# Kernel tuning notes

Measured on AMD Instinct MI355X. Metric: run time of the kernel, lower is better.

## Reference

```python
import jax, jax.numpy as jnp
import numpy as np

BATCH, N_FEATURES, D_MODEL = 8192, 8192, 1024


def setup_inputs() -> dict:
    key = jax.random.key(0)
    kx, kw = jax.random.split(key)
    # x: sparse feature activations in the original (COO); dense uniform here.
    x = jax.random.uniform(kx, (BATCH, N_FEATURES), dtype=jnp.float32)
    # Xavier-normal init for W_tr [n_features, d_model].
    std = float(np.sqrt(2.0 / (N_FEATURES + D_MODEL)))
    W_tr = jax.random.normal(kw, (N_FEATURES, D_MODEL), dtype=jnp.float32) * std
    bias = jnp.zeros((N_FEATURES,), dtype=jnp.float32)
    return {"x": x, "W_tr": W_tr, "bias": bias}


def reference(x, W_tr, bias):
    # h = x @ W_tr              : [B, n_features] @ [n_features, d_model] -> [B, d_model]
    # out = relu(h @ W_tr.T + b): [B, d_model] @ [d_model, n_features] -> [B, n_features]
    h = jnp.einsum("bf,fd->bd", x, W_tr)
    return jax.nn.relu(jnp.einsum("bd,fd->bf", h, W_tr) + bias)
```

## Files before the change

kernel.cpp:

```cpp
#include <hip/hip_runtime.h>
#include <hip/hip_bf16.h>
#include <stdint.h>

#define BATCH  8192
#define NFEAT  8192
#define DMODEL 1024

typedef unsigned short u16;
typedef __attribute__((ext_vector_type(8))) short  short8;
typedef __attribute__((ext_vector_type(4))) float  f32x4;

__device__ __forceinline__ u16 f2b(float f) {
    uint32_t u = __float_as_uint(f);
    u += 0x7fffu + ((u >> 16) & 1u);
    return (u16)(u >> 16);
}

__device__ __forceinline__ void gld16(const u16* g, void* l) {
    __builtin_amdgcn_global_load_lds(
        (const __attribute__((address_space(1))) void*)(uintptr_t)g,
        (__attribute__((address_space(3))) void*)(uint32_t)(uintptr_t)l,
        16, 0, 0);
}


__global__ void cvt_x_kernel(const float* __restrict__ x, u16* __restrict__ xb) {
    int i = blockIdx.x * blockDim.x + threadIdx.x;
    const float4* xv = (const float4*)x;
    float4 a = xv[2 * i];
    float4 b = xv[2 * i + 1];
    union { u16 u[8]; uint4 v; } o;
    o.u[0] = f2b(a.x); o.u[1] = f2b(a.y); o.u[2] = f2b(a.z); o.u[3] = f2b(a.w);
    o.u[4] = f2b(b.x); o.u[5] = f2b(b.y); o.u[6] = f2b(b.z); o.u[7] = f2b(b.w);
    ((uint4*)xb)[i] = o.v;
}

__global__ void cvt_w_kernel(const float* __restrict__ W,
                             u16* __restrict__ wb, u16* __restrict__ wt) {
    __shared__ u16 tile[64][65];
    const int f0 = blockIdx.x * 64;
    const int d0 = blockIdx.y * 64;
    const int t  = threadIdx.x;
#pragma unroll
    for (int rep = 0; rep < 16; ++rep) {
        int idx = rep * 256 + t;
        int r = idx >> 6, c = idx & 63;
        float v = W[(size_t)(f0 + r) * DMODEL + d0 + c];
        u16 u = f2b(v);
        tile[r][c] = u;
        wb[(size_t)(f0 + r) * DMODEL + d0 + c] = u;
    }
    __syncthreads();
#pragma unroll
    for (int rep = 0; rep < 16; ++rep) {
        int idx = rep * 256 + t;
        int r = idx >> 6, c = idx & 63;
        wt[(size_t)(d0 + r) * NFEAT + f0 + c] = tile[c][r];
    }
}

#define SYNC_IN()  do { __builtin_amdgcn_sched_barrier(0); __builtin_amdgcn_s_barrier(); \
                        asm volatile("s_waitcnt lgkmcnt(0)" ::: "memory");               \
                        __builtin_amdgcn_sched_barrier(0); } while (0)
#define SYNC_OUT() do { __builtin_amdgcn_s_setprio(0); __builtin_amdgcn_sched_barrier(0); \
                        __builtin_amdgcn_s_barrier(); } while (0)

__global__ __launch_bounds__(512, 2)
void gemm1_8phase(const u16* __restrict__ A, const u16* __restrict__ B,
                  u16* __restrict__ H, int N, int K) {
    const int NT = K >> 6;
    __shared__ __align__(1024) char lds[98304];
    const int BOFF = 65536;

    const int tid  = threadIdx.x;
    const int lane = tid & 63;
    const int wave = tid >> 6;
    const int wm   = wave >> 2;
    const int wn   = wave & 3;

    const int nwg = gridDim.x;
    const int swz = (blockIdx.x & 7) * (nwg >> 3) + (blockIdx.x >> 3);
    const int ntn = N >> 7;
    const int tm0 = (swz / ntn) << 8;
    const int tn0 = (swz % ntn) << 7;

    const int srl = lane >> 2;
    const int sch = (lane & 3) ^ (((lane >> 5) & 1) << 1);
    const int scol  = (wave & 1) * 32 + sch * 8;
    const int srow0 = (wave >> 1) * 16 + srl;

    const u16* pa[2][2];
    pa[0][0] = A + (size_t)(tm0 + srow0)            * K + scol;
    pa[0][1] = A + (size_t)(tm0 + srow0 + 64)       * K + scol;
    pa[1][0] = A + (size_t)(tm0 + 128 + srow0)      * K + scol;
    pa[1][1] = A + (size_t)(tm0 + 128 + srow0 + 64) * K + scol;
    const u16* pb[2];
    pb[0] = B + (size_t)(tn0 + srow0)      * K + scol;
    pb[1] = B + (size_t)(tn0 + srow0 + 64) * K + scol;

    auto STAGE_A = [&](int tau, int half) {
        if (tau < NT) {
            char* d = lds + (tau & 1) * 32768 + half * 16384 + wave * 1024;
            gld16(pa[half][0] + (size_t)tau * 64, d);
            gld16(pa[half][1] + (size_t)tau * 64, d + 8192);
        }
    };
    auto STAGE_B = [&](int tau) {
        if (tau < NT) {
            char* d = lds + BOFF + (tau & 1) * 16384 + wave * 1024;
            gld16(pb[0] + (size_t)tau * 64, d);
            gld16(pb[1] + (size_t)tau * 64, d + 8192);
        }
    };

    const int l15 = lane & 15, lhi = lane >> 4;
    const int pch = lhi ^ (((lane >> 3) & 1) << 1);
    const int lof = l15 * 64 + pch * 16;

    short8 a[4][2];
    short8 b[2][2];
    f32x4  acc[8][2] = {};

    const char* Ab;
    const char* Bb;
    auto LDA_ = [&](int mh) {
#pragma unroll
        for (int fm = 0; fm < 4; ++fm)
#pragma unroll
            for (int ks = 0; ks < 2; ++ks)
                a[fm][ks] = *(const short8*)(Ab + ((mh * 4 + fm) * 2 + ks) * 1024);
    };
    auto LDB_ = [&](int nh) {
#pragma unroll
        for (int ks = 0; ks < 2; ++ks)
            b[nh][ks] = *(const short8*)(Bb + (nh * 2 + ks) * 1024);
    };
    auto MMA_ = [&](int mh, int nh) {
#pragma unroll
        for (int ks = 0; ks < 2; ++ks)
#pragma unroll
            for (int fm = 0; fm < 4; ++fm)
                acc[mh * 4 + fm][nh] = __builtin_amdgcn_mfma_f32_16x16x32_bf16(
                    a[fm][ks], b[nh][ks], acc[mh * 4 + fm][nh], 0, 0, 0);
    };

    STAGE_A(0, 0); STAGE_A(0, 1); STAGE_B(0); STAGE_B(1);
    asm volatile("s_waitcnt vmcnt(2)" ::: "memory");
    __builtin_amdgcn_s_barrier();

    for (int t = 0; t < NT; ++t) {
        Ab = lds + (t & 1) * 32768 + wm * 16384 + lof;
        Bb = lds + BOFF + (t & 1) * 16384 + wn * 4096 + lof;

        LDA_(0); LDB_(0);
        STAGE_A(t + 1, 0);
        SYNC_IN();
        __builtin_amdgcn_s_setprio(1);
        MMA_(0, 0);
        SYNC_OUT();

        LDB_(1);
        STAGE_A(t + 1, 1);
        SYNC_IN();
        __builtin_amdgcn_s_setprio(1);
        MMA_(0, 1);
        SYNC_OUT();

        LDA_(1);
        STAGE_B(t + 2);
        SYNC_IN();
        __builtin_amdgcn_s_setprio(1);
        MMA_(1, 1);
        SYNC_OUT();

        __builtin_amdgcn_sched_barrier(0);
        __builtin_amdgcn_s_barrier();
        __builtin_amdgcn_s_setprio(1);
        MMA_(1, 0);
        __builtin_amdgcn_s_setprio(0);
        __builtin_amdgcn_sched_barrier(0);
        if (t < NT - 2)       asm volatile("s_waitcnt vmcnt(2)" ::: "memory");
        else if (t == NT - 2) asm volatile("s_waitcnt vmcnt(0)" ::: "memory");
        __builtin_amdgcn_s_barrier();
    }

    const int orow = tm0 + wm * 128;
    const int ocol = tn0 + wn * 32;
#pragma unroll
    for (int fm = 0; fm < 8; ++fm) {
        const int row0 = orow + fm * 16 + lhi * 4;
#pragma unroll
        for (int nh = 0; nh < 2; ++nh) {
            const int col = ocol + nh * 16 + l15;
#pragma unroll
            for (int r = 0; r < 4; ++r)
                H[(size_t)(row0 + r) * N + col] = f2b(acc[fm][nh][r]);
        }
    }
}

__global__ __launch_bounds__(512, 2)
void gemm2_8phase(const u16* __restrict__ A, const u16* __restrict__ B,
                  float* __restrict__ O, const float* __restrict__ bias,
                  int N, int K) {
    const int NT = K >> 6;
    __shared__ __align__(1024) char lds[131072];
    const int BOFF = 65536;

    const int tid  = threadIdx.x;
    const int lane = tid & 63;
    const int wave = tid >> 6;
    const int wm   = wave >> 2;
    const int wn   = wave & 3;

    const int nwg = gridDim.x;
    const int swz = (blockIdx.x & 7) * (nwg >> 3) + (blockIdx.x >> 3);
    const int ntn = N >> 8;
    const int tm0 = (swz / ntn) << 8;
    const int tn0 = (swz % ntn) << 8;

    const int srl = lane >> 2;
    const int sch = (lane & 3) ^ (((lane >> 5) & 1) << 1);
    const int scol  = (wave & 1) * 32 + sch * 8;
    const int srow0 = (wave >> 1) * 16 + srl;

    const u16* pa[2][2];
    const u16* pb[2][2];
    pa[0][0] = A + (size_t)(tm0 + srow0)       * K + scol;
    pa[0][1] = A + (size_t)(tm0 + srow0 + 64)  * K + scol;
    pa[1][0] = A + (size_t)(tm0 + 128 + srow0)      * K + scol;
    pa[1][1] = A + (size_t)(tm0 + 128 + srow0 + 64) * K + scol;
    pb[0][0] = B + (size_t)(tn0 + srow0)       * K + scol;
    pb[0][1] = B + (size_t)(tn0 + srow0 + 64)  * K + scol;
    pb[1][0] = B + (size_t)(tn0 + 128 + srow0)      * K + scol;
    pb[1][1] = B + (size_t)(tn0 + 128 + srow0 + 64) * K + scol;

    auto STAGE = [&](int tau, int isB, int half) {
        if (tau < NT) {
            char* d = lds + (isB ? BOFF : 0) + (tau & 1) * 32768 + half * 16384 + wave * 1024;
            const u16* p0 = (isB ? pb[half][0] : pa[half][0]) + (size_t)tau * 64;
            const u16* p1 = (isB ? pb[half][1] : pa[half][1]) + (size_t)tau * 64;
            gld16(p0, d);
            gld16(p1, d + 8192);
        }
    };

    const int l15 = lane & 15, lhi = lane >> 4;
    const int pch = lhi ^ (((lane >> 3) & 1) << 1);
    const int lof = l15 * 64 + pch * 16;

    short8 a[4][2];
    short8 b[4][2];
    f32x4  acc[8][4] = {};

    const char* Ab;
    const char* Bb;
    auto LDA_ = [&](int mh) {
#pragma unroll
        for (int fm = 0; fm < 4; ++fm)
#pragma unroll
            for (int ks = 0; ks < 2; ++ks)
                a[fm][ks] = *(const short8*)(Ab + ((mh * 4 + fm) * 2 + ks) * 1024);
    };
    auto LDB_ = [&](int nh) {
#pragma unroll
        for (int fn = 0; fn < 2; ++fn)
#pragma unroll
            for (int ks = 0; ks < 2; ++ks)
                b[nh * 2 + fn][ks] = *(const short8*)(Bb + (((wn & 1) * 4 + nh * 2 + fn) * 2 + ks) * 1024);
    };
    auto MMA_ = [&](int mh, int nh) {
#pragma unroll
        for (int ks = 0; ks < 2; ++ks)
#pragma unroll
            for (int fm = 0; fm < 4; ++fm)
#pragma unroll
                for (int fn = 0; fn < 2; ++fn)
                    acc[mh * 4 + fm][nh * 2 + fn] = __builtin_amdgcn_mfma_f32_16x16x32_bf16(
                        a[fm][ks], b[nh * 2 + fn][ks], acc[mh * 4 + fm][nh * 2 + fn], 0, 0, 0);
    };

    STAGE(0, 0, 0); STAGE(0, 0, 1); STAGE(0, 1, 0); STAGE(0, 1, 1);
    STAGE(1, 1, 0); STAGE(1, 1, 1);
    asm volatile("s_waitcnt vmcnt(4)" ::: "memory");
    __builtin_amdgcn_s_barrier();

    for (int t = 0; t < NT; ++t) {
        Ab = lds + (t & 1) * 32768 + wm * 16384 + lof;
        Bb = lds + BOFF + (t & 1) * 32768 + (wn >> 1) * 16384 + lof;

        LDA_(0); LDB_(0);
        STAGE(t + 1, 0, 0);
        asm volatile("s_waitcnt lgkmcnt(8)" ::: "memory");
        SYNC_IN();
        __builtin_amdgcn_s_setprio(1);
        MMA_(0, 0);
        SYNC_OUT();

        LDB_(1);
        STAGE(t + 1, 0, 1);
        SYNC_IN();
        __builtin_amdgcn_s_setprio(1);
        MMA_(0, 1);
        SYNC_OUT();

        LDA_(1);
        STAGE(t + 2, 1, 0);
        SYNC_IN();
        __builtin_amdgcn_s_setprio(1);
        MMA_(1, 1);
        SYNC_OUT();

        STAGE(t + 2, 1, 1);
        __builtin_amdgcn_sched_barrier(0);
        __builtin_amdgcn_s_barrier();
        asm volatile("s_waitcnt lgkmcnt(0)" ::: "memory");
        __builtin_amdgcn_sched_barrier(0);
        __builtin_amdgcn_s_setprio(1);
        MMA_(1, 0);
        __builtin_amdgcn_s_setprio(0);
        __builtin_amdgcn_sched_barrier(0);
        if (t < NT - 2)       asm volatile("s_waitcnt vmcnt(4)" ::: "memory");
        else if (t == NT - 2) asm volatile("s_waitcnt vmcnt(0)" ::: "memory");
        __builtin_amdgcn_s_barrier();
    }

    const int orow = tm0 + wm * 128;
    const int ocol = tn0 + wn * 64;
    float bv[4];
#pragma unroll
    for (int fn = 0; fn < 4; ++fn) bv[fn] = bias[ocol + fn * 16 + l15];
#pragma unroll
    for (int fm = 0; fm < 8; ++fm) {
        const int row0 = orow + fm * 16 + lhi * 4;
#pragma unroll
        for (int fn = 0; fn < 4; ++fn) {
            const int col = ocol + fn * 16 + l15;
#pragma unroll
            for (int r = 0; r < 4; ++r) {
                float v = acc[fm][fn][r] + bv[fn];
                O[(size_t)(row0 + r) * N + col] = v > 0.f ? v : 0.f;
            }
        }
    }
}


extern "C" void kernel_launch(void* const* d_in, const int* in_sizes, int n_in,
                              void* d_out, int out_size, void* d_ws, size_t ws_size,
                              hipStream_t stream) {
    const float* x    = (const float*)d_in[0];
    const float* W    = (const float*)d_in[1];
    const float* bias = (const float*)d_in[2];
    float* out = (float*)d_out;

    char* ws = (char*)d_ws;
    u16* xb = (u16*)ws;
    u16* wt = (u16*)(ws + 134217728);
    u16* wb = (u16*)(ws + 134217728 + 16777216);
    u16* hb = (u16*)(ws + 134217728 + 2 * 16777216);

    cvt_x_kernel<<<(BATCH * NFEAT / 8) / 256, 256, 0, stream>>>(x, xb);
    cvt_w_kernel<<<dim3(NFEAT / 64, DMODEL / 64), 256, 0, stream>>>(W, wb, wt);

    gemm1_8phase<<<dim3((BATCH / 256) * (DMODEL / 128)), 512, 0, stream>>>(
        xb, wt, hb, DMODEL, NFEAT);

    gemm2_8phase<<<dim3((BATCH / 256) * (NFEAT / 256)), 512, 0, stream>>>(
        hb, wb, out, bias, NFEAT, DMODEL);
}
```

Baseline: 407.5 us.

## Triple-buffer A tiles with prefetch distance two and stage gemm1 output through LDS

```diff
diff --git a/kernel.cpp b/kernel.cpp
--- a/kernel.cpp
+++ b/kernel.cpp
@@ -69,8 +69,8 @@
 void gemm1_8phase(const u16* __restrict__ A, const u16* __restrict__ B,
                   u16* __restrict__ H, int N, int K) {
     const int NT = K >> 6;
-    __shared__ __align__(1024) char lds[98304];
-    const int BOFF = 65536;
+    __shared__ __align__(1024) char lds[131072];
+    const int BOFF = 98304;
 
     const int tid  = threadIdx.x;
     const int lane = tid & 63;
@@ -100,7 +100,7 @@
 
     auto STAGE_A = [&](int tau, int half) {
         if (tau < NT) {
-            char* d = lds + (tau & 1) * 32768 + half * 16384 + wave * 1024;
+            char* d = lds + (tau % 3) * 32768 + half * 16384 + wave * 1024;
             gld16(pa[half][0] + (size_t)tau * 64, d);
             gld16(pa[half][1] + (size_t)tau * 64, d + 8192);
         }
@@ -144,23 +144,24 @@
                     a[fm][ks], b[nh][ks], acc[mh * 4 + fm][nh], 0, 0, 0);
     };
 
-    STAGE_A(0, 0); STAGE_A(0, 1); STAGE_B(0); STAGE_B(1);
-    asm volatile("s_waitcnt vmcnt(2)" ::: "memory");
+    STAGE_A(0, 0); STAGE_A(0, 1); STAGE_B(0);
+    STAGE_A(1, 0); STAGE_A(1, 1); STAGE_B(1);
+    asm volatile("s_waitcnt vmcnt(6)" ::: "memory");
     __builtin_amdgcn_s_barrier();
 
     for (int t = 0; t < NT; ++t) {
-        Ab = lds + (t & 1) * 32768 + wm * 16384 + lof;
+        Ab = lds + (t % 3) * 32768 + wm * 16384 + lof;
         Bb = lds + BOFF + (t & 1) * 16384 + wn * 4096 + lof;
 
         LDA_(0); LDB_(0);
-        STAGE_A(t + 1, 0);
+        STAGE_A(t + 2, 0);
         SYNC_IN();
         __builtin_amdgcn_s_setprio(1);
         MMA_(0, 0);
         SYNC_OUT();
 
         LDB_(1);
-        STAGE_A(t + 1, 1);
+        STAGE_A(t + 2, 1);
         SYNC_IN();
         __builtin_amdgcn_s_setprio(1);
         MMA_(0, 1);
@@ -179,23 +180,30 @@
         MMA_(1, 0);
         __builtin_amdgcn_s_setprio(0);
         __builtin_amdgcn_sched_barrier(0);
-        if (t < NT - 2)       asm volatile("s_waitcnt vmcnt(2)" ::: "memory");
+        if (t < NT - 2)       asm volatile("s_waitcnt vmcnt(6)" ::: "memory");
         else if (t == NT - 2) asm volatile("s_waitcnt vmcnt(0)" ::: "memory");
         __builtin_amdgcn_s_barrier();
     }
 
-    const int orow = tm0 + wm * 128;
-    const int ocol = tn0 + wn * 32;
-#pragma unroll
-    for (int fm = 0; fm < 8; ++fm) {
-        const int row0 = orow + fm * 16 + lhi * 4;
+    u16* lu = (u16*)lds;
+#pragma unroll
+    for (int fm = 0; fm < 8; ++fm)
 #pragma unroll
         for (int nh = 0; nh < 2; ++nh) {
-            const int col = ocol + nh * 16 + l15;
+            const int col  = wn * 32 + nh * 16 + l15;
+            const int row0 = wm * 128 + fm * 16 + lhi * 4;
 #pragma unroll
             for (int r = 0; r < 4; ++r)
-                H[(size_t)(row0 + r) * N + col] = f2b(acc[fm][nh][r]);
-        }
+                lu[(row0 + r) * 128 + col] = f2b(acc[fm][nh][r]);
+        }
+    __syncthreads();
+    const uint4* ls = (const uint4*)lds;
+#pragma unroll
+    for (int s = 0; s < 8; ++s) {
+        int i = s * 512 + tid;
+        int row = i >> 4;
+        int col = (i & 15) * 8;
+        *(uint4*)(H + (size_t)(tm0 + row) * N + (tn0 + col)) = ls[i];
     }
 }
 
@@ -204,8 +212,8 @@
                   float* __restrict__ O, const float* __restrict__ bias,
                   int N, int K) {
     const int NT = K >> 6;
-    __shared__ __align__(1024) char lds[131072];
-    const int BOFF = 65536;
+    __shared__ __align__(1024) char lds[163840];
+    const int BOFF = 98304;
 
     const int tid  = threadIdx.x;
     const int lane = tid & 63;
@@ -235,13 +243,18 @@
     pb[1][0] = B + (size_t)(tn0 + 128 + srow0)      * K + scol;
     pb[1][1] = B + (size_t)(tn0 + 128 + srow0 + 64) * K + scol;
 
-    auto STAGE = [&](int tau, int isB, int half) {
+    auto STAGE_A = [&](int tau, int half) {
         if (tau < NT) {
-            char* d = lds + (isB ? BOFF : 0) + (tau & 1) * 32768 + half * 16384 + wave * 1024;
-            const u16* p0 = (isB ? pb[half][0] : pa[half][0]) + (size_t)tau * 64;
-            const u16* p1 = (isB ? pb[half][1] : pa[half][1]) + (size_t)tau * 64;
-            gld16(p0, d);
-            gld16(p1, d + 8192);
+            char* d = lds + (tau % 3) * 32768 + half * 16384 + wave * 1024;
+            gld16(pa[half][0] + (size_t)tau * 64, d);
+            gld16(pa[half][1] + (size_t)tau * 64, d + 8192);
+        }
+    };
+    auto STAGE_B = [&](int tau, int half) {
+        if (tau < NT) {
+            char* d = lds + BOFF + (tau & 1) * 32768 + half * 16384 + wave * 1024;
+            gld16(pb[half][0] + (size_t)tau * 64, d);
+            gld16(pb[half][1] + (size_t)tau * 64, d + 8192);
         }
     };
 
@@ -280,17 +293,17 @@
                         a[fm][ks], b[nh * 2 + fn][ks], acc[mh * 4 + fm][nh * 2 + fn], 0, 0, 0);
     };
 
-    STAGE(0, 0, 0); STAGE(0, 0, 1); STAGE(0, 1, 0); STAGE(0, 1, 1);
-    STAGE(1, 1, 0); STAGE(1, 1, 1);
-    asm volatile("s_waitcnt vmcnt(4)" ::: "memory");
+    STAGE_A(0, 0); STAGE_A(0, 1); STAGE_B(0, 0); STAGE_B(0, 1);
+    STAGE_A(1, 0); STAGE_A(1, 1); STAGE_B(1, 0); STAGE_B(1, 1);
+    asm volatile("s_waitcnt vmcnt(8)" ::: "memory");
     __builtin_amdgcn_s_barrier();
 
     for (int t = 0; t < NT; ++t) {
-        Ab = lds + (t & 1) * 32768 + wm * 16384 + lof;
+        Ab = lds + (t % 3) * 32768 + wm * 16384 + lof;
         Bb = lds + BOFF + (t & 1) * 32768 + (wn >> 1) * 16384 + lof;
 
         LDA_(0); LDB_(0);
-        STAGE(t + 1, 0, 0);
+        STAGE_A(t + 2, 0);
         asm volatile("s_waitcnt lgkmcnt(8)" ::: "memory");
         SYNC_IN();
         __builtin_amdgcn_s_setprio(1);
@@ -298,20 +311,20 @@
         SYNC_OUT();
 
         LDB_(1);
-        STAGE(t + 1, 0, 1);
+        STAGE_A(t + 2, 1);
         SYNC_IN();
         __builtin_amdgcn_s_setprio(1);
         MMA_(0, 1);
         SYNC_OUT();
 
         LDA_(1);
-        STAGE(t + 2, 1, 0);
+        STAGE_B(t + 2, 0);
         SYNC_IN();
         __builtin_amdgcn_s_setprio(1);
         MMA_(1, 1);
         SYNC_OUT();
 
-        STAGE(t + 2, 1, 1);
+        STAGE_B(t + 2, 1);
         __builtin_amdgcn_sched_barrier(0);
         __builtin_amdgcn_s_barrier();
         asm volatile("s_waitcnt lgkmcnt(0)" ::: "memory");
@@ -320,7 +333,7 @@
         MMA_(1, 0);
         __builtin_amdgcn_s_setprio(0);
         __builtin_amdgcn_sched_barrier(0);
-        if (t < NT - 2)       asm volatile("s_waitcnt vmcnt(4)" ::: "memory");
+        if (t < NT - 2)       asm volatile("s_waitcnt vmcnt(8)" ::: "memory");
         else if (t == NT - 2) asm volatile("s_waitcnt vmcnt(0)" ::: "memory");
         __builtin_amdgcn_s_barrier();
     }
```

Measured after the change: 384.7 us. 1.06x faster.
